# Performance work log

Measured on AMD Instinct MI355X. Metric: run time of the kernel, lower is better.

## Reference

```python
import jax, jax.numpy as jnp
import numpy as np
import math

N_HEAD = 16
EPS = 1e-5
GELU_C = math.sqrt(2.0 / math.pi)

def _layernorm(v, w):
    # LN with weight only (bias=None), matching the module's quirky constructor
    mu = jnp.mean(v, axis=-1, keepdims=True)
    var = jnp.mean(jnp.square(v - mu), axis=-1, keepdims=True)
    return (v - mu) * jax.lax.rsqrt(var + EPS) * w

def _new_gelu(x):
    return 0.5 * x * (1.0 + jnp.tanh(GELU_C * (x + 0.044715 * x ** 3)))

def setup_inputs() -> dict:
    key = jax.random.key(0)
    k1, k2, k3, k4 = jax.random.split(key, 4)
    B, T, C = 2, 2048, 2048
    x = jax.random.normal(k1, (B, T, C), dtype=jnp.float32)
    w_qkv = jax.random.normal(k2, (C, 3 * C), dtype=jnp.float32) * 0.02
    w1 = jax.random.normal(k3, (C, 4 * C), dtype=jnp.float32) * 0.02
    w2 = jax.random.normal(k4, (4 * C, C), dtype=jnp.float32) * 0.02
    ln_w = jnp.ones((C,), dtype=jnp.float32)
    return {"x": x, "w_qkv": w_qkv, "w1": w1, "w2": w2, "ln_w": ln_w}

def reference(x, w_qkv, w1, w2, ln_w):
    B, T, C = x.shape
    H = N_HEAD
    D = C // H
    # --- attention branch (pre-LN, shared ln weight) ---
    h = _layernorm(x, ln_w)
    qkv = h @ w_qkv  # [B,T,3C]
    q, k, v = jnp.split(qkv, 3, axis=-1)
    q = q.reshape(B, T, H, D)
    k = k.reshape(B, T, H, D)
    v = v.reshape(B, T, H, D)
    scale = 1.0 / math.sqrt(D)
    att = jnp.einsum('bthd,bshd->bhts', q, k) * scale  # [B,H,T,T]
    causal = jnp.tril(jnp.ones((T, T), dtype=bool))
    att = jnp.where(causal, att, -jnp.inf)
    att = jax.nn.softmax(att, axis=-1)
    attn_out = jnp.einsum('bhts,bshd->bthd', att, v).reshape(B, T, C)
    x = x + attn_out  # note: no output projection in this module
    # --- MLP branch (same ln weight reused) ---
    h2 = _layernorm(x, ln_w)
    mlp = _new_gelu(h2 @ w1) @ w2
    return x + mlp
```

## Files before the change

kernel.cpp:

```cpp
#include <hip/hip_runtime.h>
#include <hip/hip_bf16.h>
#include <math.h>

typedef __bf16 BF16;
typedef __attribute__((ext_vector_type(8))) __bf16 bf16x8;
typedef __attribute__((ext_vector_type(4))) float f32x4;

__device__ __forceinline__ void gld_lds16(const void* g, void* l) {
    __builtin_amdgcn_global_load_lds(
        (__attribute__((address_space(1))) void*)(const void*)g,
        (__attribute__((address_space(3))) void*)l, 16, 0, 0);
}

template <int N> __device__ __forceinline__ void vmwait() {
    if constexpr (N == 0) asm volatile("s_waitcnt vmcnt(0)" ::: "memory");
    else if constexpr (N == 2) asm volatile("s_waitcnt vmcnt(2)" ::: "memory");
    else if constexpr (N == 3) asm volatile("s_waitcnt vmcnt(3)" ::: "memory");
    else if constexpr (N == 4) asm volatile("s_waitcnt vmcnt(4)" ::: "memory");
    else if constexpr (N == 6) asm volatile("s_waitcnt vmcnt(6)" ::: "memory");
    else if constexpr (N == 8) asm volatile("s_waitcnt vmcnt(8)" ::: "memory");
}

__device__ __forceinline__ void barrier_() {
    asm volatile("" ::: "memory");
    __builtin_amdgcn_s_barrier();
    asm volatile("" ::: "memory");
}

__global__ __launch_bounds__(256) void lnorm(const float* __restrict__ x,
                                             const float* __restrict__ w,
                                             BF16* __restrict__ out) {
    const int row = blockIdx.x, tid = threadIdx.x;
    const float* xr = x + (size_t)row * 2048;
    float4 a = *(const float4*)(xr + tid * 8);
    float4 b = *(const float4*)(xr + tid * 8 + 4);
    float s1 = a.x + a.y + a.z + a.w + b.x + b.y + b.z + b.w;
    float s2 = a.x*a.x + a.y*a.y + a.z*a.z + a.w*a.w +
               b.x*b.x + b.y*b.y + b.z*b.z + b.w*b.w;
    #pragma unroll
    for (int off = 32; off; off >>= 1) {
        s1 += __shfl_xor(s1, off);
        s2 += __shfl_xor(s2, off);
    }
    __shared__ float red[8];
    const int l = tid & 63, wv = tid >> 6;
    if (l == 0) { red[wv] = s1; red[4 + wv] = s2; }
    __syncthreads();
    s1 = red[0] + red[1] + red[2] + red[3];
    s2 = red[4] + red[5] + red[6] + red[7];
    const float mean = s1 * (1.0f / 2048.0f);
    const float var  = s2 * (1.0f / 2048.0f) - mean * mean;
    const float rstd = rsqrtf(var + 1e-5f);
    float4 wa = *(const float4*)(w + tid * 8);
    float4 wb = *(const float4*)(w + tid * 8 + 4);
    bf16x8 o;
    o[0] = (BF16)((a.x - mean) * rstd * wa.x);
    o[1] = (BF16)((a.y - mean) * rstd * wa.y);
    o[2] = (BF16)((a.z - mean) * rstd * wa.z);
    o[3] = (BF16)((a.w - mean) * rstd * wa.w);
    o[4] = (BF16)((b.x - mean) * rstd * wb.x);
    o[5] = (BF16)((b.y - mean) * rstd * wb.y);
    o[6] = (BF16)((b.z - mean) * rstd * wb.z);
    o[7] = (BF16)((b.w - mean) * rstd * wb.w);
    *(bf16x8*)(out + (size_t)row * 2048 + tid * 8) = o;
}

__global__ __launch_bounds__(256) void wtrans(const float* __restrict__ W,
                                              BF16* __restrict__ Wt,
                                              int K, int N) {
    __shared__ BF16 tile[32][33];
    const int n0 = blockIdx.x * 32, k0 = blockIdx.y * 32;
    const int tx = threadIdx.x, ty = threadIdx.y;
    #pragma unroll
    for (int i = 0; i < 4; i++)
        tile[ty + 8 * i][tx] = (BF16)W[(size_t)(k0 + ty + 8 * i) * N + n0 + tx];
    __syncthreads();
    #pragma unroll
    for (int i = 0; i < 4; i++)
        Wt[(size_t)(n0 + ty + 8 * i) * K + k0 + tx] = tile[tx][ty + 8 * i];
}

__global__ __launch_bounds__(256) void vtrans(const BF16* __restrict__ qkv,
                                              BF16* __restrict__ vT) {
    __shared__ BF16 tile[32][33];
    const int t0 = blockIdx.x * 32, d0 = blockIdx.y * 32, bh = blockIdx.z;
    const int b = bh >> 4, h = bh & 15;
    const int tx = threadIdx.x, ty = threadIdx.y;
    const BF16* src = qkv + (size_t)b * 2048 * 6144 + 4096 + h * 128;
    #pragma unroll
    for (int i = 0; i < 4; i++)
        tile[ty + 8 * i][tx] = src[(size_t)(t0 + ty + 8 * i) * 6144 + d0 + tx];
    __syncthreads();
    BF16* dst = vT + (size_t)bh * 128 * 2048;
    #pragma unroll
    for (int i = 0; i < 4; i++)
        dst[(size_t)(d0 + ty + 8 * i) * 2048 + t0 + tx] = tile[tx][ty + 8 * i];
}

#define STAGE_A(SB, TS) do { \
    gld_lds16(gA + (size_t)(TS) * 32, lA + (SB) * ABUF); \
    if (LA == 2) gld_lds16(gA + (size_t)(TS) * 32 + (size_t)128 * K, \
                           lA + (SB) * ABUF + 4096); \
} while (0)

#define STAGE_B(SB, TS) do { \
    gld_lds16(gB + (size_t)(TS) * 32, lB + (SB) * BBUF); \
    if (LB == 2) gld_lds16(gB + (size_t)(TS) * 32 + (size_t)128 * K, \
                           lB + (SB) * BBUF + 4096); \
} while (0)

#define TILE(BUF, TS, DS, VM) do { \
    bf16x8 af[MR], bf[NPN]; \
    _Pragma("unroll") \
    for (int m = 0; m < MR; ++m) \
        af[m] = *(const bf16x8*)&As[(BUF) * ABUF + aoff + m * 512]; \
    _Pragma("unroll") \
    for (int n = 0; n < NPN; ++n) \
        bf[n] = *(const bf16x8*)&Bs[(BUF) * BBUF + boff + n * 512]; \
    if (DS) STAGE_A(((BUF) + 3) & 3, TS); \
    if (NPH == 1) { if (DS) STAGE_B(((BUF) + 3) & 3, TS); vmwait<(VM)>(); } \
    barrier_(); \
    __builtin_amdgcn_s_setprio(1); \
    _Pragma("unroll") \
    for (int m = 0; m < MR; ++m) \
      _Pragma("unroll") \
      for (int n = 0; n < NPN; ++n) \
        acc[m][n] = __builtin_amdgcn_mfma_f32_16x16x32_bf16(af[m], bf[n], acc[m][n], 0, 0, 0); \
    __builtin_amdgcn_s_setprio(0); \
    barrier_(); \
    if (NPH == 2) { \
      bf16x8 bf2[NPN]; \
      _Pragma("unroll") \
      for (int n = 0; n < NPN; ++n) \
          bf2[n] = *(const bf16x8*)&Bs[(BUF) * BBUF + boff + (NPN + n) * 512]; \
      if (DS) STAGE_B(((BUF) + 3) & 3, TS); \
      vmwait<(VM)>(); \
      barrier_(); \
      __builtin_amdgcn_s_setprio(1); \
      _Pragma("unroll") \
      for (int m = 0; m < MR; ++m) \
        _Pragma("unroll") \
        for (int n = 0; n < NPN; ++n) \
          acc[m][NPN + n] = __builtin_amdgcn_mfma_f32_16x16x32_bf16(af[m], bf2[n], acc[m][NPN + n], 0, 0, 0); \
      __builtin_amdgcn_s_setprio(0); \
      barrier_(); \
    } \
} while (0)

template <int MODE, int BM, int BN, int WM, int WN>
__global__ __launch_bounds__(512) void gemm8(const BF16* __restrict__ A,
                                             const BF16* __restrict__ Bt,
                                             void* __restrict__ out,
                                             const float* __restrict__ resid,
                                             int M, int N, int K) {
    constexpr int MR  = BM / WM / 16;
    constexpr int NR  = BN / WN / 16;
    constexpr int NPH = (MR * NR) / 16;
    constexpr int NPN = NR / NPH;
    constexpr int LA  = BM / 128;
    constexpr int LB  = BN / 128;
    constexpr int L   = LA + LB;
    constexpr int ABUF = BM * 32;
    constexpr int BBUF = BN * 32;
    (void)M;

    extern __shared__ char smem[];
    BF16* const As = (BF16*)smem;
    BF16* const Bs = As + 4 * ABUF;

    const int tid = threadIdx.x, l = tid & 63, w = tid >> 6;
    const int wm = w / WN, wn = w % WN;
    const int g = l >> 4, c = l & 15;
    const int fa = (c >> 1) & 3;

    const int NBX = N / BN;
    const int cpx = (int)gridDim.x >> 3;
    const int bid = (int)blockIdx.x;
    const int wg  = (bid & 7) * cpx + (bid >> 3);
    const int m0 = (wg / NBX) * BM, n0 = (wg % NBX) * BN;

    const int r0 = tid >> 2;
    const int klog = (tid & 3) ^ ((r0 >> 1) & 3);
    const BF16* const gA = A  + (size_t)(m0 + r0) * K + klog * 8;
    const BF16* const gB = Bt + (size_t)(n0 + r0) * K + klog * 8;
    BF16* const lA = As + w * 512;
    BF16* const lB = Bs + w * 512;

    const int aoff = (wm * (BM / WM) + c) * 32 + ((g ^ fa) << 3);
    const int boff = (wn * (BN / WN) + c) * 32 + ((g ^ fa) << 3);

    f32x4 acc[MR][NR] = {};

    STAGE_A(0, 0); STAGE_B(0, 0);
    STAGE_A(1, 1); STAGE_B(1, 1);
    STAGE_A(2, 2); STAGE_B(2, 2);
    vmwait<2 * L>();
    barrier_();

    const int NT = K >> 5;
    for (int t = 0; t < NT - 4; t += 4) {
        TILE(0, t + 3, true, 2 * L);
        TILE(1, t + 4, true, 2 * L);
        TILE(2, t + 5, true, 2 * L);
        TILE(3, t + 6, true, 2 * L);
    }
    TILE(0, NT - 1, true, 2 * L);
    TILE(1, 0, false, L);
    TILE(2, 0, false, 0);
    TILE(3, 0, false, -1);

    #pragma unroll
    for (int mi = 0; mi < MR; mi++)
      #pragma unroll
      for (int ni = 0; ni < NR; ni++)
        #pragma unroll
        for (int j = 0; j < 4; j++) {
            const int row = m0 + wm * (BM / WM) + mi * 16 + g * 4 + j;
            const int col = n0 + wn * (BN / WN) + ni * 16 + c;
            const float v = acc[mi][ni][j];
            const size_t idx = (size_t)row * N + col;
            if (MODE == 0) {
                ((BF16*)out)[idx] = (BF16)v;
            } else if (MODE == 1) {
                const float t2 = v + 0.044715f * v * v * v;
                const float s = 1.0f / (1.0f + __expf(-1.5957691216057308f * t2));
                ((BF16*)out)[idx] = (BF16)(v * s);
            } else {
                ((float*)out)[idx] = resid[idx] + v;
            }
        }
}

__global__ __launch_bounds__(256) void attn(const BF16* __restrict__ qkv,
                                            const BF16* __restrict__ vT,
                                            const float* __restrict__ x,
                                            float* __restrict__ x2) {
    __shared__ BF16 Ks[64 * 128];
    __shared__ BF16 Vs[128 * 64];
    __shared__ BF16 Ps[4][16 * 72];
    const int tid = threadIdx.x, l = tid & 63, w = tid >> 6;
    const int g = l >> 4, c = l & 15;
    const int qb = 31 - (int)blockIdx.x, bh = blockIdx.y;
    const int b = bh >> 4, h = bh & 15;
    const int q0 = qb * 64;
    const int xr = (c & 7) << 4;

    const BF16* qbase = qkv + (size_t)b * 2048 * 6144 + h * 128;
    const char* kbase = (const char*)(qbase + 2048);
    const char* vbase = (const char*)(vT + (size_t)bh * 128 * 2048);

    bf16x8 qf[4];
    {
        const BF16* qrow = qbase + (size_t)(q0 + w * 16 + c) * 6144 + g * 8;
        #pragma unroll
        for (int kc = 0; kc < 4; kc++) qf[kc] = *(const bf16x8*)(qrow + kc * 32);
    }

    float m[4]    = {-1e30f, -1e30f, -1e30f, -1e30f};
    float lsum[4] = {0.f, 0.f, 0.f, 0.f};
    f32x4 O[8] = {};
    const float scale = 0.08838834764831845f;

    for (int kt = 0; kt <= qb; ++kt) {
        const int k0 = kt * 64;
        __syncthreads();
        #pragma unroll
        for (int s = 0; s < 4; ++s) {
            const int rK = (w * 4 + s) * 4 + (l >> 4);
            const int cK = ((l & 15) * 16) ^ ((rK & 7) << 4);
            gld_lds16(kbase + (size_t)(k0 + rK) * 12288 + cK,
                      &Ks[(w * 4 + s) * 512]);
            const int rV = (w * 4 + s) * 8 + (l >> 3);
            const int cV = ((l & 7) * 16) ^ ((rV & 7) << 4);
            gld_lds16(vbase + (size_t)rV * 4096 + (size_t)k0 * 2 + cV,
                      &Vs[(w * 4 + s) * 512]);
        }
        __syncthreads();

        f32x4 s4[4] = {};
        #pragma unroll
        for (int ni = 0; ni < 4; ni++)
            #pragma unroll
            for (int kc = 0; kc < 4; kc++) {
                const bf16x8 kf = *(const bf16x8*)((const char*)Ks +
                    (ni * 16 + c) * 256 + ((kc * 64 + g * 16) ^ xr));
                s4[ni] = __builtin_amdgcn_mfma_f32_16x16x32_bf16(
                    qf[kc], kf, s4[ni], 0, 0, 0);
            }

        const bool maskt = (kt == qb);
        float sv[4][4];
        #pragma unroll
        for (int ni = 0; ni < 4; ni++)
            #pragma unroll
            for (int j = 0; j < 4; j++) {
                const float v = s4[ni][j] * scale;
                sv[ni][j] = (!maskt || (ni * 16 + c <= w * 16 + g * 4 + j))
                          ? v : -1e30f;
            }

        float sf[4];
        #pragma unroll
        for (int j = 0; j < 4; j++) {
            float tm = fmaxf(fmaxf(sv[0][j], sv[1][j]), fmaxf(sv[2][j], sv[3][j]));
            tm = fmaxf(tm, __shfl_xor(tm, 1));
            tm = fmaxf(tm, __shfl_xor(tm, 2));
            tm = fmaxf(tm, __shfl_xor(tm, 4));
            tm = fmaxf(tm, __shfl_xor(tm, 8));
            const float mn = fmaxf(m[j], tm);
            sf[j] = __expf(m[j] - mn);
            m[j] = mn;
        }

        float rs[4] = {0.f, 0.f, 0.f, 0.f};
        #pragma unroll
        for (int ni = 0; ni < 4; ni++)
            #pragma unroll
            for (int j = 0; j < 4; j++) {
                const float p = __expf(sv[ni][j] - m[j]);
                rs[j] += p;
                Ps[w][(g * 4 + j) * 72 + ni * 16 + c] = (BF16)p;
            }
        #pragma unroll
        for (int j = 0; j < 4; j++) {
            float t = rs[j];
            t += __shfl_xor(t, 1);
            t += __shfl_xor(t, 2);
            t += __shfl_xor(t, 4);
            t += __shfl_xor(t, 8);
            lsum[j] = lsum[j] * sf[j] + t;
        }
        #pragma unroll
        for (int dn = 0; dn < 8; dn++)
            #pragma unroll
            for (int j = 0; j < 4; j++) O[dn][j] *= sf[j];

        bf16x8 pa[2];
        #pragma unroll
        for (int ks = 0; ks < 2; ks++)
            pa[ks] = *(const bf16x8*)((const char*)Ps[w] +
                         c * 144 + ks * 64 + g * 16);
        #pragma unroll
        for (int dn = 0; dn < 8; dn++)
            #pragma unroll
            for (int ks = 0; ks < 2; ks++) {
                const bf16x8 vf = *(const bf16x8*)((const char*)Vs +
                    (dn * 16 + c) * 128 + ((ks * 64 + g * 16) ^ xr));
                O[dn] = __builtin_amdgcn_mfma_f32_16x16x32_bf16(
                    pa[ks], vf, O[dn], 0, 0, 0);
            }
    }

    float inv[4];
    #pragma unroll
    for (int j = 0; j < 4; j++) inv[j] = 1.0f / lsum[j];
    #pragma unroll
    for (int dn = 0; dn < 8; dn++)
        #pragma unroll
        for (int j = 0; j < 4; j++) {
            const int t   = q0 + w * 16 + g * 4 + j;
            const int col = h * 128 + dn * 16 + c;
            const size_t idx = ((size_t)b * 2048 + t) * 2048 + col;
            x2[idx] = x[idx] + O[dn][j] * inv[j];
        }
}

extern "C" void kernel_launch(void* const* d_in, const int* in_sizes, int n_in,
                              void* d_out, int out_size, void* d_ws, size_t ws_size,
                              hipStream_t stream) {
    const float* x     = (const float*)d_in[0];
    const float* w_qkv = (const float*)d_in[1];
    const float* w1    = (const float*)d_in[2];
    const float* w2    = (const float*)d_in[3];
    const float* ln_w  = (const float*)d_in[4];
    float* out = (float*)d_out;

    char* ws = (char*)d_ws;
    BF16* h_buf = (BF16*)ws;  ws += (size_t)4096 * 2048 * 2;
    BF16* qkvb  = (BF16*)ws;  ws += (size_t)4096 * 6144 * 2;
    BF16* vTb   = (BF16*)ws;  ws += (size_t)32 * 128 * 2048 * 2;
    BF16* wqkvT = (BF16*)ws;  ws += (size_t)6144 * 2048 * 2;
    BF16* w1T   = (BF16*)ws;  ws += (size_t)8192 * 2048 * 2;
    BF16* w2T   = (BF16*)ws;  ws += (size_t)2048 * 8192 * 2;
    BF16* mlp1  = (BF16*)ws;  ws += (size_t)4096 * 8192 * 2;

    hipFuncSetAttribute((const void*)&gemm8<0, 256, 256, 2, 4>,
                        hipFuncAttributeMaxDynamicSharedMemorySize, 131072);
    hipFuncSetAttribute((const void*)&gemm8<1, 256, 256, 2, 4>,
                        hipFuncAttributeMaxDynamicSharedMemorySize, 131072);
    hipFuncSetAttribute((const void*)&gemm8<2, 256, 128, 4, 2>,
                        hipFuncAttributeMaxDynamicSharedMemorySize, 98304);

    lnorm<<<4096, 256, 0, stream>>>(x, ln_w, h_buf);
    wtrans<<<dim3(192, 64), dim3(32, 8), 0, stream>>>(w_qkv, wqkvT, 2048, 6144);
    gemm8<0, 256, 256, 2, 4><<<384, 512, 131072, stream>>>(
        h_buf, wqkvT, qkvb, nullptr, 4096, 6144, 2048);
    vtrans<<<dim3(64, 4, 32), dim3(32, 8), 0, stream>>>(qkvb, vTb);
    attn<<<dim3(32, 32), 256, 0, stream>>>(qkvb, vTb, x, out);

    lnorm<<<4096, 256, 0, stream>>>(out, ln_w, h_buf);
    wtrans<<<dim3(256, 64), dim3(32, 8), 0, stream>>>(w1, w1T, 2048, 8192);
    gemm8<1, 256, 256, 2, 4><<<512, 512, 131072, stream>>>(
        h_buf, w1T, mlp1, nullptr, 4096, 8192, 2048);
    wtrans<<<dim3(64, 256), dim3(32, 8), 0, stream>>>(w2, w2T, 8192, 2048);
    gemm8<2, 256, 128, 4, 2><<<256, 512, 98304, stream>>>(
        mlp1, w2T, out, out, 4096, 2048, 8192);
}
```

Baseline: 644.1 us.

## Double-buffer K/V tiles and pair causal query blocks in attention

The attention kernel now double-buffers K and V tiles in LDS, issuing the next tile's async global-to-LDS loads before computing the current one, and waits with vmcnt. Each workgroup handles two query blocks (pair and 31-pair) so causal work is balanced, cutting the grid to 512 blocks. Block ids are remapped with an XCD-style swizzle so neighbouring heads share a die. This doubles LDS use per block and may reduce occupancy, and it relies on the hand-placed waitcnt and barrier ordering being correct.

New measurement: 556.0 us. 1.16x faster.

```diff
diff --git a/kernel.cpp b/kernel.cpp
--- a/kernel.cpp
+++ b/kernel.cpp
@@ -235,134 +235,151 @@
                                             const BF16* __restrict__ vT,
                                             const float* __restrict__ x,
                                             float* __restrict__ x2) {
-    __shared__ BF16 Ks[64 * 128];
-    __shared__ BF16 Vs[128 * 64];
+    __shared__ BF16 Ks[2][64 * 128];
+    __shared__ BF16 Vs[2][128 * 64];
     __shared__ BF16 Ps[4][16 * 72];
     const int tid = threadIdx.x, l = tid & 63, w = tid >> 6;
     const int g = l >> 4, c = l & 15;
-    const int qb = 31 - (int)blockIdx.x, bh = blockIdx.y;
+    const int bid = (int)blockIdx.x;
+    const int wg = (bid & 7) * 64 + (bid >> 3);
+    const int pair = wg & 15, bh = wg >> 4;
     const int b = bh >> 4, h = bh & 15;
-    const int q0 = qb * 64;
     const int xr = (c & 7) << 4;
 
     const BF16* qbase = qkv + (size_t)b * 2048 * 6144 + h * 128;
     const char* kbase = (const char*)(qbase + 2048);
     const char* vbase = (const char*)(vT + (size_t)bh * 128 * 2048);
 
-    bf16x8 qf[4];
-    {
-        const BF16* qrow = qbase + (size_t)(q0 + w * 16 + c) * 6144 + g * 8;
-        #pragma unroll
-        for (int kc = 0; kc < 4; kc++) qf[kc] = *(const bf16x8*)(qrow + kc * 32);
-    }
-
-    float m[4]    = {-1e30f, -1e30f, -1e30f, -1e30f};
-    float lsum[4] = {0.f, 0.f, 0.f, 0.f};
-    f32x4 O[8] = {};
-    const float scale = 0.08838834764831845f;
-
-    for (int kt = 0; kt <= qb; ++kt) {
-        const int k0 = kt * 64;
-        __syncthreads();
+    auto STAGE = [&](int bb, int k0) {
         #pragma unroll
         for (int s = 0; s < 4; ++s) {
             const int rK = (w * 4 + s) * 4 + (l >> 4);
             const int cK = ((l & 15) * 16) ^ ((rK & 7) << 4);
             gld_lds16(kbase + (size_t)(k0 + rK) * 12288 + cK,
-                      &Ks[(w * 4 + s) * 512]);
+                      &Ks[bb][(w * 4 + s) * 512]);
             const int rV = (w * 4 + s) * 8 + (l >> 3);
             const int cV = ((l & 7) * 16) ^ ((rV & 7) << 4);
             gld_lds16(vbase + (size_t)rV * 4096 + (size_t)k0 * 2 + cV,
-                      &Vs[(w * 4 + s) * 512]);
+                      &Vs[bb][(w * 4 + s) * 512]);
         }
-        __syncthreads();
-
-        f32x4 s4[4] = {};
+    };
+
+    const float scale = 0.08838834764831845f;
+
+    #pragma unroll 1
+    for (int seg = 0; seg < 2; ++seg) {
+        const int qb = seg ? 31 - pair : pair;
+        const int q0 = qb * 64;
+
+        bf16x8 qf[4];
+        {
+            const BF16* qrow = qbase + (size_t)(q0 + w * 16 + c) * 6144 + g * 8;
+            #pragma unroll
+            for (int kc = 0; kc < 4; kc++)
+                qf[kc] = *(const bf16x8*)(qrow + kc * 32);
+        }
+        float m[4]    = {-1e30f, -1e30f, -1e30f, -1e30f};
+        float lsum[4] = {0.f, 0.f, 0.f, 0.f};
+        f32x4 O[8] = {};
+
+        STAGE(0, 0);
+        #pragma unroll 1
+        for (int kt = 0; kt <= qb; ++kt) {
+            if (kt < qb) { STAGE((kt + 1) & 1, (kt + 1) * 64); vmwait<8>(); }
+            else vmwait<0>();
+            barrier_();
+            const char* KsB = (const char*)Ks[kt & 1];
+            const char* VsB = (const char*)Vs[kt & 1];
+
+            f32x4 s4[4] = {};
+            #pragma unroll
+            for (int ni = 0; ni < 4; ni++)
+                #pragma unroll
+                for (int kc = 0; kc < 4; kc++) {
+                    const bf16x8 kf = *(const bf16x8*)(KsB +
+                        (ni * 16 + c) * 256 + ((kc * 64 + g * 16) ^ xr));
+                    s4[ni] = __builtin_amdgcn_mfma_f32_16x16x32_bf16(
+                        qf[kc], kf, s4[ni], 0, 0, 0);
+                }
+
+            const bool maskt = (kt == qb);
+            float sv[4][4];
+            #pragma unroll
+            for (int ni = 0; ni < 4; ni++)
+                #pragma unroll
+                for (int j = 0; j < 4; j++) {
+                    const float v = s4[ni][j] * scale;
+                    sv[ni][j] = (!maskt || (ni * 16 + c <= w * 16 + g * 4 + j))
+                              ? v : -1e30f;
+                }
+
+            float sf[4];
+            #pragma unroll
+            for (int j = 0; j < 4; j++) {
+                float tm = fmaxf(fmaxf(sv[0][j], sv[1][j]),
+                                 fmaxf(sv[2][j], sv[3][j]));
+                tm = fmaxf(tm, __shfl_xor(tm, 1));
+                tm = fmaxf(tm, __shfl_xor(tm, 2));
+                tm = fmaxf(tm, __shfl_xor(tm, 4));
+                tm = fmaxf(tm, __shfl_xor(tm, 8));
+                const float mn = fmaxf(m[j], tm);
+                sf[j] = __expf(m[j] - mn);
+                m[j] = mn;
+            }
+
+            float rs[4] = {0.f, 0.f, 0.f, 0.f};
+            #pragma unroll
+            for (int ni = 0; ni < 4; ni++)
+                #pragma unroll
+                for (int j = 0; j < 4; j++) {
+                    const float p = __expf(sv[ni][j] - m[j]);
+                    rs[j] += p;
+                    Ps[w][(g * 4 + j) * 72 + ni * 16 + c] = (BF16)p;
+                }
+            #pragma unroll
+            for (int j = 0; j < 4; j++) {
+                float t = rs[j];
+                t += __shfl_xor(t, 1);
+                t += __shfl_xor(t, 2);
+                t += __shfl_xor(t, 4);
+                t += __shfl_xor(t, 8);
+                lsum[j] = lsum[j] * sf[j] + t;
+            }
+            #pragma unroll
+            for (int dn = 0; dn < 8; dn++)
+                #pragma unroll
+                for (int j = 0; j < 4; j++) O[dn][j] *= sf[j];
+
+            bf16x8 pa[2];
+            #pragma unroll
+            for (int ks = 0; ks < 2; ks++)
+                pa[ks] = *(const bf16x8*)((const char*)Ps[w] +
+                             c * 144 + ks * 64 + g * 16);
+            #pragma unroll
+            for (int dn = 0; dn < 8; dn++)
+                #pragma unroll
+                for (int ks = 0; ks < 2; ks++) {
+                    const bf16x8 vf = *(const bf16x8*)(VsB +
+                        (dn * 16 + c) * 128 + ((ks * 64 + g * 16) ^ xr));
+                    O[dn] = __builtin_amdgcn_mfma_f32_16x16x32_bf16(
+                        pa[ks], vf, O[dn], 0, 0, 0);
+                }
+            barrier_();
+        }
+
+        float inv[4];
         #pragma unroll
-        for (int ni = 0; ni < 4; ni++)
-            #pragma unroll
-            for (int kc = 0; kc < 4; kc++) {
-                const bf16x8 kf = *(const bf16x8*)((const char*)Ks +
-                    (ni * 16 + c) * 256 + ((kc * 64 + g * 16) ^ xr));
-                s4[ni] = __builtin_amdgcn_mfma_f32_16x16x32_bf16(
-                    qf[kc], kf, s4[ni], 0, 0, 0);
-            }
-
-        const bool maskt = (kt == qb);
-        float sv[4][4];
-        #pragma unroll
-        for (int ni = 0; ni < 4; ni++)
-            #pragma unroll
-            for (int j = 0; j < 4; j++) {
-                const float v = s4[ni][j] * scale;
-                sv[ni][j] = (!maskt || (ni * 16 + c <= w * 16 + g * 4 + j))
-                          ? v : -1e30f;
-            }
-
-        float sf[4];
-        #pragma unroll
-        for (int j = 0; j < 4; j++) {
-            float tm = fmaxf(fmaxf(sv[0][j], sv[1][j]), fmaxf(sv[2][j], sv[3][j]));
-            tm = fmaxf(tm, __shfl_xor(tm, 1));
-            tm = fmaxf(tm, __shfl_xor(tm, 2));
-            tm = fmaxf(tm, __shfl_xor(tm, 4));
-            tm = fmaxf(tm, __shfl_xor(tm, 8));
-            const float mn = fmaxf(m[j], tm);
-            sf[j] = __expf(m[j] - mn);
-            m[j] = mn;
-        }
-
-        float rs[4] = {0.f, 0.f, 0.f, 0.f};
-        #pragma unroll
-        for (int ni = 0; ni < 4; ni++)
-            #pragma unroll
-            for (int j = 0; j < 4; j++) {
-                const float p = __expf(sv[ni][j] - m[j]);
-                rs[j] += p;
-                Ps[w][(g * 4 + j) * 72 + ni * 16 + c] = (BF16)p;
-            }
-        #pragma unroll
-        for (int j = 0; j < 4; j++) {
-            float t = rs[j];
-            t += __shfl_xor(t, 1);
-            t += __shfl_xor(t, 2);
-            t += __shfl_xor(t, 4);
-            t += __shfl_xor(t, 8);
-            lsum[j] = lsum[j] * sf[j] + t;
-        }
+        for (int j = 0; j < 4; j++) inv[j] = 1.0f / lsum[j];
         #pragma unroll
         for (int dn = 0; dn < 8; dn++)
             #pragma unroll
-            for (int j = 0; j < 4; j++) O[dn][j] *= sf[j];
-
-        bf16x8 pa[2];
-        #pragma unroll
-        for (int ks = 0; ks < 2; ks++)
-            pa[ks] = *(const bf16x8*)((const char*)Ps[w] +
-                         c * 144 + ks * 64 + g * 16);
-        #pragma unroll
-        for (int dn = 0; dn < 8; dn++)
-            #pragma unroll
-            for (int ks = 0; ks < 2; ks++) {
-                const bf16x8 vf = *(const bf16x8*)((const char*)Vs +
-                    (dn * 16 + c) * 128 + ((ks * 64 + g * 16) ^ xr));
-                O[dn] = __builtin_amdgcn_mfma_f32_16x16x32_bf16(
-                    pa[ks], vf, O[dn], 0, 0, 0);
+            for (int j = 0; j < 4; j++) {
+                const int t   = q0 + w * 16 + g * 4 + j;
+                const int col = h * 128 + dn * 16 + c;
+                const size_t idx = ((size_t)b * 2048 + t) * 2048 + col;
+                x2[idx] = x[idx] + O[dn][j] * inv[j];
             }
     }
-
-    float inv[4];
-    #pragma unroll
-    for (int j = 0; j < 4; j++) inv[j] = 1.0f / lsum[j];
-    #pragma unroll
-    for (int dn = 0; dn < 8; dn++)
-        #pragma unroll
-        for (int j = 0; j < 4; j++) {
-            const int t   = q0 + w * 16 + g * 4 + j;
-            const int col = h * 128 + dn * 16 + c;
-            const size_t idx = ((size_t)b * 2048 + t) * 2048 + col;
-            x2[idx] = x[idx] + O[dn][j] * inv[j];
-        }
 }
 
 extern "C" void kernel_launch(void* const* d_in, const int* in_sizes, int n_in,
@@ -396,7 +413,7 @@
     gemm8<0, 256, 256, 2, 4><<<384, 512, 131072, stream>>>(
         h_buf, wqkvT, qkvb, nullptr, 4096, 6144, 2048);
     vtrans<<<dim3(64, 4, 32), dim3(32, 8), 0, stream>>>(qkvb, vTb);
-    attn<<<dim3(32, 32), 256, 0, stream>>>(qkvb, vTb, x, out);
+    attn<<<512, 256, 0, stream>>>(qkvb, vTb, x, out);
 
     lnorm<<<4096, 256, 0, stream>>>(out, ln_w, h_buf);
     wtrans<<<dim3(256, 64), dim3(32, 8), 0, stream>>>(w1, w1T, 2048, 8192);
```
